# Performance work log

Hardware: AMD Instinct MI355X
Metric: run time of the kernel (lower is better)

The kernel has to match this reference:

```python
import jax, jax.numpy as jnp
import numpy as np

N_HEADS = 8
WINDOW = 7

def _conv1x1(x, W, b):
    # x: [B,H,W,C]; 1x1 conv == per-pixel matmul
    return jnp.einsum('bhwc,cd->bhwd', x, W) + b

def _to_heads(t, nh):
    # [B,H,W,C] -> channels-first reshape [B, nh, C//nh, H*W] (matches tf transpose+reshape)
    B, H, W, C = t.shape
    return jnp.transpose(t, (0, 3, 1, 2)).reshape(B, nh, C // nh, H * W)

def setup_inputs() -> dict:
    key = jax.random.key(0)
    ks = jax.random.split(key, 8)
    B, H, W, C = 2, 56, 56, 256
    x = jax.random.normal(ks[0], (B, H, W, C), dtype=jnp.float32)
    s = 1.0 / np.sqrt(C)
    Wq = jax.random.normal(ks[1], (C, C), dtype=jnp.float32) * s
    bq = jnp.zeros((C,), dtype=jnp.float32)
    Wk = jax.random.normal(ks[2], (C, C), dtype=jnp.float32) * s
    bk = jnp.zeros((C,), dtype=jnp.float32)
    Wv = jax.random.normal(ks[3], (C, C), dtype=jnp.float32) * s
    bv = jnp.zeros((C,), dtype=jnp.float32)
    # original initializes gamma to 0 (output == x); use small nonzero so the
    # attention path is observable in outputs/grads
    gamma = jax.random.normal(ks[4], (1,), dtype=jnp.float32) * 0.1
    return {"x": x, "Wq": Wq, "bq": bq, "Wk": Wk, "bk": bk, "Wv": Wv, "bv": bv, "gamma": gamma}

def reference(x, Wq, bq, Wk, bk, Wv, bv, gamma):
    B, H, W, C = x.shape
    p = WINDOW // 2
    xp = jnp.pad(x, ((0, 0), (p, p), (p, p), (0, 0)), mode='reflect')  # [B,Hp,Wp,C]
    q = _to_heads(_conv1x1(x, Wq, bq), N_HEADS)    # [B,nh,dk,HW]
    k = _to_heads(_conv1x1(xp, Wk, bk), N_HEADS)   # [B,nh,dk,HpWp]
    v = _to_heads(_conv1x1(xp, Wv, bv), N_HEADS)   # [B,nh,dk,HpWp]
    energy = jnp.einsum('bhdq,bhdk->bhqk', q, k)   # [B,nh,HW,HpWp]
    attn = jax.nn.softmax(energy, axis=-1)
    out = jnp.einsum('bhdk,bhqk->bhdq', v, attn)   # [B,nh,dk,HW]
    out = out.reshape(B, C, H, W).transpose(0, 2, 3, 1)
    return gamma * out + x
```

## Files before the change

### kernel.cpp

```cpp
#include <hip/hip_runtime.h>

typedef unsigned short u16;
typedef float f32x4 __attribute__((ext_vector_type(4)));
typedef short bf16x8 __attribute__((ext_vector_type(8)));
typedef short bf16x4 __attribute__((ext_vector_type(4)));

__device__ __forceinline__ u16 f2bf(float f) {
    unsigned u = __float_as_uint(f);
    u = (u + 0x7FFFu + ((u >> 16) & 1u)) >> 16;
    return (u16)u;
}

#define LOG2E 1.4426950408889634f

#if __has_builtin(__builtin_amdgcn_exp2f)
__device__ __forceinline__ float exp2_fast(float x) { return __builtin_amdgcn_exp2f(x); }
#else
__device__ __forceinline__ float exp2_fast(float x) { return __expf(x * 0.6931471805599453f); }
#endif

__device__ __forceinline__ unsigned pack2bf(float a, float b) {
    unsigned ua = __float_as_uint(a) + 0x8000u;
    unsigned ub = __float_as_uint(b) + 0x8000u;
#if __has_builtin(__builtin_amdgcn_perm)
    return __builtin_amdgcn_perm(ub, ua, 0x07060302u);
#else
    return ((ua >> 16) & 0xFFFFu) | (ub & 0xFFFF0000u);
#endif
}

#if __has_builtin(__builtin_amdgcn_cvt_pk_bf16_f32)
typedef __bf16 bf2_t __attribute__((ext_vector_type(2)));
__device__ __forceinline__ unsigned cvtpk(float a, float b) {
    bf2_t r = __builtin_amdgcn_cvt_pk_bf16_f32(a, b);
    return __builtin_bit_cast(unsigned, r);
}
#else
__device__ __forceinline__ unsigned cvtpk(float a, float b) { return pack2bf(a, b); }
#endif

__device__ __forceinline__ bf16x4 bc4(uint2 u) { return __builtin_bit_cast(bf16x4, u); }
__device__ __forceinline__ bf16x8 bc8(uint4 u) { return __builtin_bit_cast(bf16x8, u); }

#if __has_builtin(__builtin_amdgcn_global_load_lds)
typedef const __attribute__((address_space(1))) void* as1cv;
typedef __attribute__((address_space(3))) void* as3v;
__device__ __forceinline__ void dma16(const void* g, void* lds_base, int lane) {
    __builtin_amdgcn_global_load_lds((as1cv)g, (as3v)lds_base, 16, 0, 0);
}
#else
__device__ __forceinline__ void dma16(const void* g, void* lds_base, int lane) {
    *(uint4*)((char*)lds_base + lane * 16) = *(const uint4*)g;
}
#endif

#if __has_builtin(__builtin_amdgcn_mfma_f32_16x16x16bf16_1k)
__device__ __forceinline__ f32x4 pv_mfma(bf16x4 a, bf16x4 b, f32x4 c) {
    return __builtin_amdgcn_mfma_f32_16x16x16bf16_1k(a, b, c, 0, 0, 0);
}
#elif __has_builtin(__builtin_amdgcn_mfma_f32_16x16x16_bf16)
__device__ __forceinline__ f32x4 pv_mfma(bf16x4 a, bf16x4 b, f32x4 c) {
    return __builtin_amdgcn_mfma_f32_16x16x16_bf16(a, b, c, 0, 0, 0);
}
#else
__device__ __forceinline__ f32x4 pv_mfma(bf16x4 a, bf16x4 b, f32x4 c) {
    bf16x8 a8 = {a[0], a[1], a[2], a[3], 0, 0, 0, 0};
    bf16x8 b8 = {b[0], b[1], b[2], b[3], 0, 0, 0, 0};
    return __builtin_amdgcn_mfma_f32_16x16x32_bf16(a8, b8, c, 0, 0, 0);
}
#endif

#define BB 2
#define HH 56
#define CC 256
#define NH 8
#define DK 32
#define SQ 3136
#define HP 62
#define SK 3844
#define VT_STRIDE 3856

#define WS_Q    0
#define WS_K    1605632
#define WS_VT   3573760
#define WS_LB   5548032

#define NZERO_F4 413952

#define BSTR 40
__global__ __launch_bounds__(256, 4) void proj_kernel(const float* __restrict__ x,
                                                      const float* __restrict__ Wq,
                                                      const float* __restrict__ Wk,
                                                      const float* __restrict__ Wv,
                                                      const float* __restrict__ bq,
                                                      const float* __restrict__ bk,
                                                      const float* __restrict__ bv,
                                                      u16* __restrict__ qout,
                                                      u16* __restrict__ kout,
                                                      u16* __restrict__ vtout,
                                                      float* __restrict__ out,
                                                      float* __restrict__ lbuf) {
    __shared__ __align__(16) u16 Bl[128 * BSTR];

    int mode  = blockIdx.y;
    int nz    = blockIdx.z;
    int mbase = blockIdx.x * 64;
    int tid = threadIdx.x;

    {
        int gid = ((blockIdx.z * 3 + blockIdx.y) * 121 + blockIdx.x) * 256 + tid;
        const int n_out4 = (SQ * BB * CC) / 4;
        for (int i = gid; i < NZERO_F4; i += 726 * 256) {
            if (i < n_out4) *(float4*)&out[i * 4] = (float4){0.f, 0.f, 0.f, 0.f};
            else            *(float4*)&lbuf[(i - n_out4) * 4] = (float4){0.f, 0.f, 0.f, 0.f};
        }
    }

    int M = (mode == 0) ? (BB * SQ) : (BB * SK);
    if (mbase >= M) return;
    int wave = tid >> 6, lane = tid & 63, quad = lane >> 4, l16 = lane & 15;

    const float* W = (mode == 0) ? Wq : ((mode == 1) ? Wk : Wv);
    const float* bias = (mode == 0) ? bq : ((mode == 1) ? bk : bv);
    float wscale = (mode == 0) ? LOG2E : 1.0f;

    int m_a = mbase + wave * 16 + l16;
    if (m_a >= M) m_a = M - 1;
    int xrow;
    if (mode == 0) {
        xrow = m_a;
    } else {
        int b = (m_a >= SK) ? 1 : 0;
        int sp = m_a - b * SK;
        int hp = sp / HP, wp = sp - hp * HP;
        int hs = hp - 3; hs = hs < 0 ? -hs : (hs >= HH ? 110 - hs : hs);
        int ws_ = wp - 3; ws_ = ws_ < 0 ? -ws_ : (ws_ >= HH ? 110 - ws_ : ws_);
        xrow = b * SQ + hs * HH + ws_;
    }
    const float* xr = x + (size_t)xrow * 256;

    int kq = tid >> 3;
    int cb = (tid & 7) * 16;

    f32x4 acc[8];
#pragma unroll
    for (int i = 0; i < 8; i++) acc[i] = (f32x4){0.f, 0.f, 0.f, 0.f};

    float4 wreg[4];
    auto wload = [&](int s) {
        const float* p = W + (size_t)(s * 32 + kq) * 256 + nz * 128 + cb;
        wreg[0] = *(const float4*)&p[0];
        wreg[1] = *(const float4*)&p[4];
        wreg[2] = *(const float4*)&p[8];
        wreg[3] = *(const float4*)&p[12];
    };

    wload(0);
    for (int s = 0; s < 8; ++s) {
        int kk = s * 32;
#pragma unroll
        for (int i = 0; i < 16; i++) {
            float v = ((const float*)wreg)[i] * wscale;
            Bl[(cb + i) * BSTR + kq] = f2bf(v);
        }
        __syncthreads();
        if (s < 7) wload(s + 1);
        float4 f0 = *(const float4*)&xr[kk + quad * 8];
        float4 f1 = *(const float4*)&xr[kk + quad * 8 + 4];
        uint4 aw = (uint4){pack2bf(f0.x, f0.y), pack2bf(f0.z, f0.w),
                           pack2bf(f1.x, f1.y), pack2bf(f1.z, f1.w)};
        bf16x8 afrag = bc8(aw);
#pragma unroll
        for (int nt = 0; nt < 8; nt++) {
            bf16x8 bfrag = *(const bf16x8*)&Bl[(nt * 16 + l16) * BSTR + quad * 8];
            acc[nt] = __builtin_amdgcn_mfma_f32_16x16x32_bf16(afrag, bfrag, acc[nt], 0, 0, 0);
        }
        __syncthreads();
    }

    int mrow_base = mbase + wave * 16 + quad * 4;
    if (mode == 2) {
#pragma unroll
        for (int nt = 0; nt < 8; nt++) {
            int c = nz * 128 + nt * 16 + l16;
            float bvv = bias[c];
#pragma unroll
            for (int p = 0; p < 4; p += 2) {
                int m = mrow_base + p;
                if (m + 1 < M) {
                    int bb = (m >= SK) ? 1 : 0;
                    int kp = m - bb * SK;
                    unsigned pk = pack2bf(acc[nt][p] + bvv, acc[nt][p + 1] + bvv);
                    *(unsigned*)&vtout[(size_t)(bb * 256 + c) * VT_STRIDE + kp] = pk;
                }
            }
        }
    } else {
#pragma unroll
        for (int r = 0; r < 4; r++) {
            int m = mrow_base + r;
            if (m >= M) continue;
#pragma unroll
            for (int nt = 0; nt < 8; nt++) {
                int c = nz * 128 + nt * 16 + l16;
                float v = acc[nt][r] + bias[c] * ((mode == 0) ? LOG2E : 1.0f);
                u16 hv = f2bf(v);
                if (mode == 0) qout[((size_t)m << 8) + c] = hv;
                else           kout[((size_t)m << 8) + c] = hv;
            }
        }
    }
}

__global__ __launch_bounds__(256, 4) void attn_kernel(const u16* __restrict__ qb,
                                                      const u16* __restrict__ kb,
                                                      const u16* __restrict__ vtb,
                                                      float* __restrict__ out,
                                                      float* __restrict__ lbuf) {
    __shared__ __align__(16) u16 S[16384];

    int tid = threadIdx.x;
    int th = tid >> 6, lane = tid & 63, quad = lane >> 4, l16 = lane & 15;
    int bh = blockIdx.y;
    int b = bh >> 3, h = bh & 7;
    int half = blockIdx.z;
    int qsub = blockIdx.x * 64;
    int rounds = half ? 15 : 16;

    bf16x8 qf[4];
#pragma unroll
    for (int i = 0; i < 4; ++i)
        qf[i] = *(const bf16x8*)&qb[((size_t)(b * SQ + qsub + i * 16 + l16) << 8) + h * 32 + quad * 8];

    const u16* kg = kb + ((size_t)(b * SK) << 8) + h * 32;
    const u16* vg = vtb + (size_t)(b * 256 + h * 32) * VT_STRIDE;

    f32x4 o[4][2], lv[4];
#pragma unroll
    for (int i = 0; i < 4; ++i) {
        o[i][0] = (f32x4){0.f,0.f,0.f,0.f};
        o[i][1] = (f32x4){0.f,0.f,0.f,0.f};
        lv[i]   = (f32x4){0.f,0.f,0.f,0.f};
    }

    short ov = (l16 == 0) ? (short)0x3F80 : (short)0;
    bf16x4 ones4 = {ov, ov, ov, ov};

    auto stage = [&](int r_ch, int buf) {
        u16* base = &S[buf * 8192];
        int kbase = (half * 16 + r_ch) * 128;
#pragma unroll
        for (int i = 0; i < 2; ++i) {
            int g = th + i * 4;
            int grow = kbase + g * 16 + (lane & 15);
            if (grow > SK - 1) grow = SK - 1;
            dma16(kg + ((size_t)grow << 8) + (lane >> 4) * 8, base + g * 512, lane);
            int col = kbase + (2 * g + (lane >> 5)) * 8;
            if (col > VT_STRIDE - 8) col = VT_STRIDE - 8;
            dma16(vg + (size_t)(lane & 31) * VT_STRIDE + col, base + 4096 + g * 512, lane);
        }
    };

    stage(0, 0);
    __syncthreads();
    stage(1, 1);

    for (int r = 0; r < rounds; ++r) {
        const u16* Kl = &S[(r & 1) * 8192];
        const u16* Vl = Kl + 4096;
        int ch = half * 16 + r;
        bool tail = (ch == 30);
#pragma unroll
        for (int tt = 0; tt < 2; ++tt) {
            int t = th + tt * 4;
            bf16x8 kf = *(const bf16x8*)&Kl[t * 512 + ((quad << 4) + l16) * 8];
            f32x4 e[4];
#pragma unroll
            for (int i = 0; i < 4; ++i)
                e[i] = __builtin_amdgcn_mfma_f32_16x16x32_bf16(kf, qf[i], (f32x4){0.f,0.f,0.f,0.f}, 0, 0, 0);
            bf16x4 pa[4];
            if (tail) {
                int kb0 = ch * 128 + t * 16 + quad * 4;
#pragma unroll
                for (int i = 0; i < 4; ++i) {
                    float p0 = (kb0 + 0) < SK ? exp2_fast(e[i][0]) : 0.f;
                    float p1 = (kb0 + 1) < SK ? exp2_fast(e[i][1]) : 0.f;
                    float p2 = (kb0 + 2) < SK ? exp2_fast(e[i][2]) : 0.f;
                    float p3 = (kb0 + 3) < SK ? exp2_fast(e[i][3]) : 0.f;
                    pa[i] = bc4((uint2){cvtpk(p0, p1), cvtpk(p2, p3)});
                }
            } else {
#pragma unroll
                for (int i = 0; i < 4; ++i) {
                    pa[i] = bc4((uint2){cvtpk(exp2_fast(e[i][0]), exp2_fast(e[i][1])),
                                        cvtpk(exp2_fast(e[i][2]), exp2_fast(e[i][3]))});
                }
            }
            int vbase = ((2 * t + (quad >> 1)) << 8) + (quad & 1) * 4;
            uint2 w0 = *(const uint2*)&Vl[vbase + l16 * 8];
            uint2 w1 = *(const uint2*)&Vl[vbase + (16 + l16) * 8];
            bf16x4 vb0 = bc4(w0), vb1 = bc4(w1);
#pragma unroll
            for (int i = 0; i < 4; ++i) {
                o[i][0] = pv_mfma(pa[i], vb0, o[i][0]);
                o[i][1] = pv_mfma(pa[i], vb1, o[i][1]);
                lv[i]   = pv_mfma(pa[i], ones4, lv[i]);
            }
        }
        __syncthreads();
        if (r + 2 < rounds) stage(r + 2, r & 1);
    }

    float* mg = (float*)&S[0];
    {
        int slot = ((th & 1) * 64 + lane) * 48;
        if (th >= 2) {
#pragma unroll
            for (int i = 0; i < 4; ++i) {
                *(f32x4*)&mg[slot + i * 8]     = o[i][0];
                *(f32x4*)&mg[slot + i * 8 + 4] = o[i][1];
                *(f32x4*)&mg[slot + 32 + i * 4] = lv[i];
            }
        }
        __syncthreads();
        if (th < 2) {
#pragma unroll
            for (int i = 0; i < 4; ++i) {
                o[i][0] += *(const f32x4*)&mg[slot + i * 8];
                o[i][1] += *(const f32x4*)&mg[slot + i * 8 + 4];
                lv[i]   += *(const f32x4*)&mg[slot + 32 + i * 4];
            }
        }
        __syncthreads();
    }
    {
        int slot = lane * 48;
        if (th == 1) {
#pragma unroll
            for (int i = 0; i < 4; ++i) {
                *(f32x4*)&mg[slot + i * 8]     = o[i][0];
                *(f32x4*)&mg[slot + i * 8 + 4] = o[i][1];
                *(f32x4*)&mg[slot + 32 + i * 4] = lv[i];
            }
        }
        __syncthreads();
        if (th == 0) {
#pragma unroll
            for (int i = 0; i < 4; ++i) {
                o[i][0] += *(const f32x4*)&mg[slot + i * 8];
                o[i][1] += *(const f32x4*)&mg[slot + i * 8 + 4];
                lv[i]   += *(const f32x4*)&mg[slot + 32 + i * 4];
            }

#pragma unroll
            for (int i = 0; i < 4; ++i) {
#pragma unroll
                for (int r2 = 0; r2 < 4; ++r2) {
                    int q = qsub + i * 16 + quad * 4 + r2;
                    size_t base = (size_t)(b * SQ + q) * 256 + h * 32;
                    atomicAdd(&out[base + l16],      o[i][0][r2]);
                    atomicAdd(&out[base + 16 + l16], o[i][1][r2]);
                    if (l16 == 0) atomicAdd(&lbuf[(b * SQ + q) * 8 + h], lv[i][r2]);
                }
            }
        }
    }
}

__global__ __launch_bounds__(256) void finalize_kernel(const float* __restrict__ x,
                                                       const float* __restrict__ gammap,
                                                       const float* __restrict__ lbuf,
                                                       float* __restrict__ out) {
    int gid = blockIdx.x * 256 + threadIdx.x;
    int row = gid >> 6;
    int c4  = (gid & 63) << 2;
    int h   = c4 >> 5;
    float g = gammap[0];
    float linv = g / lbuf[row * 8 + h];
    size_t base = (size_t)row * 256 + c4;
    float4 o = *(const float4*)&out[base];
    float4 xv = *(const float4*)&x[base];
    o.x = o.x * linv + xv.x;
    o.y = o.y * linv + xv.y;
    o.z = o.z * linv + xv.z;
    o.w = o.w * linv + xv.w;
    *(float4*)&out[base] = o;
}

extern "C" void kernel_launch(void* const* d_in, const int* in_sizes, int n_in,
                              void* d_out, int out_size, void* d_ws, size_t ws_size,
                              hipStream_t stream) {
    const float* x     = (const float*)d_in[0];
    const float* Wq    = (const float*)d_in[1];
    const float* bq    = (const float*)d_in[2];
    const float* Wk    = (const float*)d_in[3];
    const float* bk    = (const float*)d_in[4];
    const float* Wv    = (const float*)d_in[5];
    const float* bv    = (const float*)d_in[6];
    const float* gamma = (const float*)d_in[7];
    float* out = (float*)d_out;

    u16* ws   = (u16*)d_ws;
    u16* qbuf = ws + WS_Q;
    u16* kbuf = ws + WS_K;
    u16* vtb  = ws + WS_VT;
    float* lbuf = (float*)(ws + WS_LB);

    proj_kernel<<<dim3(121, 3, 2), 256, 0, stream>>>(x, Wq, Wk, Wv, bq, bk, bv,
                                                     qbuf, kbuf, vtb, out, lbuf);
    attn_kernel<<<dim3(49, 16, 2), 256, 0, stream>>>(qbuf, kbuf, vtb, out, lbuf);
    finalize_kernel<<<1568, 256, 0, stream>>>(x, gamma, lbuf, out);
}
```

Baseline: 155.7 us.

## Pretranspose weights, drop KV split and atomics, fuse finalize into attention

Adds a weight-prep kernel that converts and transposes Wq/Wk/Wv to bf16 once, so the projection kernel reads B fragments straight from global memory with no LDS staging or barriers. The attention kernel stops splitting keys into two halves, so each block processes all 31 chunks and writes the normalized, gamma-scaled residual output directly. This removes the zeroing pass, the atomics and the finalize kernel. The PV product now uses 16x16x32 MFMAs by packing two key tiles, and the row sum is computed with VALU adds instead of an extra MFMA against ones. The cost is half as many attention blocks (784) and therefore less parallelism, plus one extra small launch.

```diff
diff --git a/kernel.cpp b/kernel.cpp
--- a/kernel.cpp
+++ b/kernel.cpp
@@ -3,7 +3,7 @@
 typedef unsigned short u16;
 typedef float f32x4 __attribute__((ext_vector_type(4)));
 typedef short bf16x8 __attribute__((ext_vector_type(8)));
-typedef short bf16x4 __attribute__((ext_vector_type(4)));
+typedef u16 u16x4 __attribute__((ext_vector_type(4)));
 
 __device__ __forceinline__ u16 f2bf(float f) {
     unsigned u = __float_as_uint(f);
@@ -39,7 +39,6 @@
 __device__ __forceinline__ unsigned cvtpk(float a, float b) { return pack2bf(a, b); }
 #endif
 
-__device__ __forceinline__ bf16x4 bc4(uint2 u) { return __builtin_bit_cast(bf16x4, u); }
 __device__ __forceinline__ bf16x8 bc8(uint4 u) { return __builtin_bit_cast(bf16x8, u); }
 
 #if __has_builtin(__builtin_amdgcn_global_load_lds)
@@ -54,27 +53,8 @@
 }
 #endif
 
-#if __has_builtin(__builtin_amdgcn_mfma_f32_16x16x16bf16_1k)
-__device__ __forceinline__ f32x4 pv_mfma(bf16x4 a, bf16x4 b, f32x4 c) {
-    return __builtin_amdgcn_mfma_f32_16x16x16bf16_1k(a, b, c, 0, 0, 0);
-}
-#elif __has_builtin(__builtin_amdgcn_mfma_f32_16x16x16_bf16)
-__device__ __forceinline__ f32x4 pv_mfma(bf16x4 a, bf16x4 b, f32x4 c) {
-    return __builtin_amdgcn_mfma_f32_16x16x16_bf16(a, b, c, 0, 0, 0);
-}
-#else
-__device__ __forceinline__ f32x4 pv_mfma(bf16x4 a, bf16x4 b, f32x4 c) {
-    bf16x8 a8 = {a[0], a[1], a[2], a[3], 0, 0, 0, 0};
-    bf16x8 b8 = {b[0], b[1], b[2], b[3], 0, 0, 0, 0};
-    return __builtin_amdgcn_mfma_f32_16x16x32_bf16(a8, b8, c, 0, 0, 0);
-}
-#endif
-
 #define BB 2
 #define HH 56
-#define CC 256
-#define NH 8
-#define DK 32
 #define SQ 3136
 #define HP 62
 #define SK 3844
@@ -83,46 +63,61 @@
 #define WS_Q    0
 #define WS_K    1605632
 #define WS_VT   3573760
-#define WS_LB   5548032
-
-#define NZERO_F4 413952
-
-#define BSTR 40
+#define WS_WT   5548032
+
+__global__ __launch_bounds__(256) void wprep_kernel(const float* __restrict__ Wq,
+                                                    const float* __restrict__ Wk,
+                                                    const float* __restrict__ Wv,
+                                                    u16* __restrict__ wt,
+                                                    u16* __restrict__ vtb) {
+    __shared__ u16 T[64][72];
+    int m = blockIdx.z;
+    const float* W = (m == 0) ? Wq : ((m == 1) ? Wk : Wv);
+    float sc = (m == 0) ? LOG2E : 1.0f;
+    int kx = blockIdx.x * 64, dx = blockIdx.y * 64;
+    int tid = threadIdx.x;
+    int r16 = tid >> 4, c4 = (tid & 15) * 4;
+#pragma unroll
+    for (int p = 0; p < 4; ++p) {
+        int kr = p * 16 + r16;
+        float4 f = *(const float4*)&W[(size_t)(kx + kr) * 256 + dx + c4];
+        T[c4 + 0][kr] = f2bf(f.x * sc);
+        T[c4 + 1][kr] = f2bf(f.y * sc);
+        T[c4 + 2][kr] = f2bf(f.z * sc);
+        T[c4 + 3][kr] = f2bf(f.w * sc);
+    }
+    __syncthreads();
+#pragma unroll
+    for (int p = 0; p < 4; ++p) {
+        int dr = p * 16 + r16;
+        u16x4 v = {T[dr][c4], T[dr][c4 + 1], T[dr][c4 + 2], T[dr][c4 + 3]};
+        *(u16x4*)&wt[(size_t)m * 65536 + (size_t)(dx + dr) * 256 + kx + c4] = v;
+    }
+    if (m == 0 && blockIdx.x == 0 && blockIdx.y == 0) {
+        for (int i = tid; i < 512 * 12; i += 256) {
+            int row = i / 12, col = 3844 + (i - row * 12);
+            vtb[(size_t)row * VT_STRIDE + col] = 0;
+        }
+    }
+}
+
 __global__ __launch_bounds__(256, 4) void proj_kernel(const float* __restrict__ x,
-                                                      const float* __restrict__ Wq,
-                                                      const float* __restrict__ Wk,
-                                                      const float* __restrict__ Wv,
+                                                      const u16* __restrict__ wt,
                                                       const float* __restrict__ bq,
                                                       const float* __restrict__ bk,
                                                       const float* __restrict__ bv,
                                                       u16* __restrict__ qout,
                                                       u16* __restrict__ kout,
-                                                      u16* __restrict__ vtout,
-                                                      float* __restrict__ out,
-                                                      float* __restrict__ lbuf) {
-    __shared__ __align__(16) u16 Bl[128 * BSTR];
-
-    int mode  = blockIdx.y;
-    int nz    = blockIdx.z;
+                                                      u16* __restrict__ vtout) {
+    int mode = blockIdx.y, nz = blockIdx.z;
     int mbase = blockIdx.x * 64;
-    int tid = threadIdx.x;
-
-    {
-        int gid = ((blockIdx.z * 3 + blockIdx.y) * 121 + blockIdx.x) * 256 + tid;
-        const int n_out4 = (SQ * BB * CC) / 4;
-        for (int i = gid; i < NZERO_F4; i += 726 * 256) {
-            if (i < n_out4) *(float4*)&out[i * 4] = (float4){0.f, 0.f, 0.f, 0.f};
-            else            *(float4*)&lbuf[(i - n_out4) * 4] = (float4){0.f, 0.f, 0.f, 0.f};
-        }
-    }
-
     int M = (mode == 0) ? (BB * SQ) : (BB * SK);
     if (mbase >= M) return;
-    int wave = tid >> 6, lane = tid & 63, quad = lane >> 4, l16 = lane & 15;
-
-    const float* W = (mode == 0) ? Wq : ((mode == 1) ? Wk : Wv);
+    int tid = threadIdx.x;
+    int wave = tid >> 6, quad = (tid >> 4) & 3, l16 = tid & 15;
     const float* bias = (mode == 0) ? bq : ((mode == 1) ? bk : bv);
-    float wscale = (mode == 0) ? LOG2E : 1.0f;
+    const u16* Wm = wt + (size_t)mode * 65536 + (size_t)(nz * 128) * 256;
+    const u16* wr = Wm + (size_t)l16 * 256 + quad * 8;
 
     int m_a = mbase + wave * 16 + l16;
     if (m_a >= M) m_a = M - 1;
@@ -130,52 +125,31 @@
     if (mode == 0) {
         xrow = m_a;
     } else {
-        int b = (m_a >= SK) ? 1 : 0;
-        int sp = m_a - b * SK;
+        int bb = (m_a >= SK) ? 1 : 0;
+        int sp = m_a - bb * SK;
         int hp = sp / HP, wp = sp - hp * HP;
         int hs = hp - 3; hs = hs < 0 ? -hs : (hs >= HH ? 110 - hs : hs);
         int ws_ = wp - 3; ws_ = ws_ < 0 ? -ws_ : (ws_ >= HH ? 110 - ws_ : ws_);
-        xrow = b * SQ + hs * HH + ws_;
+        xrow = bb * SQ + hs * HH + ws_;
     }
     const float* xr = x + (size_t)xrow * 256;
 
-    int kq = tid >> 3;
-    int cb = (tid & 7) * 16;
-
     f32x4 acc[8];
 #pragma unroll
     for (int i = 0; i < 8; i++) acc[i] = (f32x4){0.f, 0.f, 0.f, 0.f};
 
-    float4 wreg[4];
-    auto wload = [&](int s) {
-        const float* p = W + (size_t)(s * 32 + kq) * 256 + nz * 128 + cb;
-        wreg[0] = *(const float4*)&p[0];
-        wreg[1] = *(const float4*)&p[4];
-        wreg[2] = *(const float4*)&p[8];
-        wreg[3] = *(const float4*)&p[12];
-    };
-
-    wload(0);
+#pragma unroll
     for (int s = 0; s < 8; ++s) {
-        int kk = s * 32;
-#pragma unroll
-        for (int i = 0; i < 16; i++) {
-            float v = ((const float*)wreg)[i] * wscale;
-            Bl[(cb + i) * BSTR + kq] = f2bf(v);
-        }
-        __syncthreads();
-        if (s < 7) wload(s + 1);
-        float4 f0 = *(const float4*)&xr[kk + quad * 8];
-        float4 f1 = *(const float4*)&xr[kk + quad * 8 + 4];
+        float4 f0 = *(const float4*)&xr[s * 32 + quad * 8];
+        float4 f1 = *(const float4*)&xr[s * 32 + quad * 8 + 4];
         uint4 aw = (uint4){pack2bf(f0.x, f0.y), pack2bf(f0.z, f0.w),
                            pack2bf(f1.x, f1.y), pack2bf(f1.z, f1.w)};
-        bf16x8 afrag = bc8(aw);
+        bf16x8 af = bc8(aw);
 #pragma unroll
         for (int nt = 0; nt < 8; nt++) {
-            bf16x8 bfrag = *(const bf16x8*)&Bl[(nt * 16 + l16) * BSTR + quad * 8];
-            acc[nt] = __builtin_amdgcn_mfma_f32_16x16x32_bf16(afrag, bfrag, acc[nt], 0, 0, 0);
-        }
-        __syncthreads();
+            bf16x8 bfrag = *(const bf16x8*)&wr[nt * 4096 + s * 32];
+            acc[nt] = __builtin_amdgcn_mfma_f32_16x16x32_bf16(af, bfrag, acc[nt], 0, 0, 0);
+        }
     }
 
     int mrow_base = mbase + wave * 16 + quad * 4;
@@ -215,17 +189,16 @@
 __global__ __launch_bounds__(256, 4) void attn_kernel(const u16* __restrict__ qb,
                                                       const u16* __restrict__ kb,
                                                       const u16* __restrict__ vtb,
-                                                      float* __restrict__ out,
-                                                      float* __restrict__ lbuf) {
+                                                      const float* __restrict__ x,
+                                                      const float* __restrict__ gammap,
+                                                      float* __restrict__ out) {
     __shared__ __align__(16) u16 S[16384];
 
     int tid = threadIdx.x;
     int th = tid >> 6, lane = tid & 63, quad = lane >> 4, l16 = lane & 15;
-    int bh = blockIdx.y;
+    int bh = blockIdx.x;
     int b = bh >> 3, h = bh & 7;
-    int half = blockIdx.z;
-    int qsub = blockIdx.x * 64;
-    int rounds = half ? 15 : 16;
+    int qsub = blockIdx.y * 64;
 
     bf16x8 qf[4];
 #pragma unroll
@@ -235,20 +208,17 @@
     const u16* kg = kb + ((size_t)(b * SK) << 8) + h * 32;
     const u16* vg = vtb + (size_t)(b * 256 + h * 32) * VT_STRIDE;
 
-    f32x4 o[4][2], lv[4];
+    f32x4 o[4][2];
+    f32x4 lacc = (f32x4){0.f, 0.f, 0.f, 0.f};
 #pragma unroll
     for (int i = 0; i < 4; ++i) {
-        o[i][0] = (f32x4){0.f,0.f,0.f,0.f};
-        o[i][1] = (f32x4){0.f,0.f,0.f,0.f};
-        lv[i]   = (f32x4){0.f,0.f,0.f,0.f};
-    }
-
-    short ov = (l16 == 0) ? (short)0x3F80 : (short)0;
-    bf16x4 ones4 = {ov, ov, ov, ov};
+        o[i][0] = (f32x4){0.f, 0.f, 0.f, 0.f};
+        o[i][1] = (f32x4){0.f, 0.f, 0.f, 0.f};
+    }
 
     auto stage = [&](int r_ch, int buf) {
         u16* base = &S[buf * 8192];
-        int kbase = (half * 16 + r_ch) * 128;
+        int kbase = r_ch * 128;
 #pragma unroll
         for (int i = 0; i < 2; ++i) {
             int g = th + i * 4;
@@ -265,62 +235,65 @@
     __syncthreads();
     stage(1, 1);
 
-    for (int r = 0; r < rounds; ++r) {
+    int tA = th, tB = th + 4;
+    int vOffA = tA * 512 + (((quad >> 1) * 32 + l16) << 3) + (quad & 1) * 4;
+    int vOffB = tB * 512 + (((quad >> 1) * 32 + l16) << 3) + (quad & 1) * 4;
+
+    for (int r = 0; r < 31; ++r) {
         const u16* Kl = &S[(r & 1) * 8192];
         const u16* Vl = Kl + 4096;
-        int ch = half * 16 + r;
-        bool tail = (ch == 30);
-#pragma unroll
-        for (int tt = 0; tt < 2; ++tt) {
-            int t = th + tt * 4;
-            bf16x8 kf = *(const bf16x8*)&Kl[t * 512 + ((quad << 4) + l16) * 8];
-            f32x4 e[4];
-#pragma unroll
-            for (int i = 0; i < 4; ++i)
-                e[i] = __builtin_amdgcn_mfma_f32_16x16x32_bf16(kf, qf[i], (f32x4){0.f,0.f,0.f,0.f}, 0, 0, 0);
-            bf16x4 pa[4];
+        bf16x8 kfA = *(const bf16x8*)&Kl[tA * 512 + lane * 8];
+        bf16x8 kfB = *(const bf16x8*)&Kl[tB * 512 + lane * 8];
+        uint2 wA0 = *(const uint2*)&Vl[vOffA];
+        uint2 wB0 = *(const uint2*)&Vl[vOffB];
+        uint2 wA1 = *(const uint2*)&Vl[vOffA + 128];
+        uint2 wB1 = *(const uint2*)&Vl[vOffB + 128];
+        bf16x8 V0 = bc8((uint4){wA0.x, wA0.y, wB0.x, wB0.y});
+        bf16x8 V1 = bc8((uint4){wA1.x, wA1.y, wB1.x, wB1.y});
+
+        f32x4 eA[4], eB[4];
+#pragma unroll
+        for (int i = 0; i < 4; ++i)
+            eA[i] = __builtin_amdgcn_mfma_f32_16x16x32_bf16(kfA, qf[i], (f32x4){0.f, 0.f, 0.f, 0.f}, 0, 0, 0);
+#pragma unroll
+        for (int i = 0; i < 4; ++i)
+            eB[i] = __builtin_amdgcn_mfma_f32_16x16x32_bf16(kfB, qf[i], (f32x4){0.f, 0.f, 0.f, 0.f}, 0, 0, 0);
+
+        bool tail = (r == 30);
+#pragma unroll
+        for (int i = 0; i < 4; ++i) {
+            float pA0 = exp2_fast(eA[i][0]), pA1 = exp2_fast(eA[i][1]);
+            float pA2 = exp2_fast(eA[i][2]), pA3 = exp2_fast(eA[i][3]);
+            float pB0 = exp2_fast(eB[i][0]), pB1 = exp2_fast(eB[i][1]);
+            float pB2 = exp2_fast(eB[i][2]), pB3 = exp2_fast(eB[i][3]);
             if (tail) {
-                int kb0 = ch * 128 + t * 16 + quad * 4;
-#pragma unroll
-                for (int i = 0; i < 4; ++i) {
-                    float p0 = (kb0 + 0) < SK ? exp2_fast(e[i][0]) : 0.f;
-                    float p1 = (kb0 + 1) < SK ? exp2_fast(e[i][1]) : 0.f;
-                    float p2 = (kb0 + 2) < SK ? exp2_fast(e[i][2]) : 0.f;
-                    float p3 = (kb0 + 3) < SK ? exp2_fast(e[i][3]) : 0.f;
-                    pa[i] = bc4((uint2){cvtpk(p0, p1), cvtpk(p2, p3)});
-                }
-            } else {
-#pragma unroll
-                for (int i = 0; i < 4; ++i) {
-                    pa[i] = bc4((uint2){cvtpk(exp2_fast(e[i][0]), exp2_fast(e[i][1])),
-                                        cvtpk(exp2_fast(e[i][2]), exp2_fast(e[i][3]))});
-                }
-            }
-            int vbase = ((2 * t + (quad >> 1)) << 8) + (quad & 1) * 4;
-            uint2 w0 = *(const uint2*)&Vl[vbase + l16 * 8];
-            uint2 w1 = *(const uint2*)&Vl[vbase + (16 + l16) * 8];
-            bf16x4 vb0 = bc4(w0), vb1 = bc4(w1);
-#pragma unroll
-            for (int i = 0; i < 4; ++i) {
-                o[i][0] = pv_mfma(pa[i], vb0, o[i][0]);
-                o[i][1] = pv_mfma(pa[i], vb1, o[i][1]);
-                lv[i]   = pv_mfma(pa[i], ones4, lv[i]);
-            }
+                int kA0 = 3840 + tA * 16 + quad * 4;
+                pA0 = (kA0 + 0 < SK) ? pA0 : 0.f;
+                pA1 = (kA0 + 1 < SK) ? pA1 : 0.f;
+                pA2 = (kA0 + 2 < SK) ? pA2 : 0.f;
+                pA3 = (kA0 + 3 < SK) ? pA3 : 0.f;
+                pB0 = 0.f; pB1 = 0.f; pB2 = 0.f; pB3 = 0.f;
+            }
+            lacc[i] += ((pA0 + pA1) + (pA2 + pA3)) + ((pB0 + pB1) + (pB2 + pB3));
+            bf16x8 pa = bc8((uint4){cvtpk(pA0, pA1), cvtpk(pA2, pA3),
+                                    cvtpk(pB0, pB1), cvtpk(pB2, pB3)});
+            o[i][0] = __builtin_amdgcn_mfma_f32_16x16x32_bf16(pa, V0, o[i][0], 0, 0, 0);
+            o[i][1] = __builtin_amdgcn_mfma_f32_16x16x32_bf16(pa, V1, o[i][1], 0, 0, 0);
         }
         __syncthreads();
-        if (r + 2 < rounds) stage(r + 2, r & 1);
+        if (r + 2 < 31) stage(r + 2, r & 1);
     }
 
     float* mg = (float*)&S[0];
     {
-        int slot = ((th & 1) * 64 + lane) * 48;
+        int slot = ((th & 1) * 64 + lane) * 40;
         if (th >= 2) {
 #pragma unroll
             for (int i = 0; i < 4; ++i) {
                 *(f32x4*)&mg[slot + i * 8]     = o[i][0];
                 *(f32x4*)&mg[slot + i * 8 + 4] = o[i][1];
-                *(f32x4*)&mg[slot + 32 + i * 4] = lv[i];
-            }
+            }
+            *(f32x4*)&mg[slot + 32] = lacc;
         }
         __syncthreads();
         if (th < 2) {
@@ -328,20 +301,20 @@
             for (int i = 0; i < 4; ++i) {
                 o[i][0] += *(const f32x4*)&mg[slot + i * 8];
                 o[i][1] += *(const f32x4*)&mg[slot + i * 8 + 4];
-                lv[i]   += *(const f32x4*)&mg[slot + 32 + i * 4];
-            }
+            }
+            lacc += *(const f32x4*)&mg[slot + 32];
         }
         __syncthreads();
     }
     {
-        int slot = lane * 48;
+        int slot = lane * 40;
         if (th == 1) {
 #pragma unroll
             for (int i = 0; i < 4; ++i) {
                 *(f32x4*)&mg[slot + i * 8]     = o[i][0];
                 *(f32x4*)&mg[slot + i * 8 + 4] = o[i][1];
-                *(f32x4*)&mg[slot + 32 + i * 4] = lv[i];
-            }
+            }
+            *(f32x4*)&mg[slot + 32] = lacc;
         }
         __syncthreads();
         if (th == 0) {
@@ -349,42 +322,30 @@
             for (int i = 0; i < 4; ++i) {
                 o[i][0] += *(const f32x4*)&mg[slot + i * 8];
                 o[i][1] += *(const f32x4*)&mg[slot + i * 8 + 4];
-                lv[i]   += *(const f32x4*)&mg[slot + 32 + i * 4];
-            }
-
+            }
+            lacc += *(const f32x4*)&mg[slot + 32];
+#pragma unroll
+            for (int c = 0; c < 4; ++c) {
+                float v = lacc[c];
+                v += __shfl_xor(v, 16);
+                v += __shfl_xor(v, 32);
+                lacc[c] = v;
+            }
+            float g = gammap[0];
 #pragma unroll
             for (int i = 0; i < 4; ++i) {
 #pragma unroll
                 for (int r2 = 0; r2 < 4; ++r2) {
+                    float l = __shfl(lacc[i], quad * 4 + r2);
+                    float scl = g / l;
                     int q = qsub + i * 16 + quad * 4 + r2;
-                    size_t base = (size_t)(b * SQ + q) * 256 + h * 32;
-                    atomicAdd(&out[base + l16],      o[i][0][r2]);
-                    atomicAdd(&out[base + 16 + l16], o[i][1][r2]);
-                    if (l16 == 0) atomicAdd(&lbuf[(b * SQ + q) * 8 + h], lv[i][r2]);
+                    size_t base = ((size_t)(b * SQ + q) << 8) + h * 32 + l16;
+                    out[base]      = o[i][0][r2] * scl + x[base];
+                    out[base + 16] = o[i][1][r2] * scl + x[base + 16];
                 }
             }
         }
     }
-}
-
-__global__ __launch_bounds__(256) void finalize_kernel(const float* __restrict__ x,
-                                                       const float* __restrict__ gammap,
-                                                       const float* __restrict__ lbuf,
-                                                       float* __restrict__ out) {
-    int gid = blockIdx.x * 256 + threadIdx.x;
-    int row = gid >> 6;
-    int c4  = (gid & 63) << 2;
-    int h   = c4 >> 5;
-    float g = gammap[0];
-    float linv = g / lbuf[row * 8 + h];
-    size_t base = (size_t)row * 256 + c4;
-    float4 o = *(const float4*)&out[base];
-    float4 xv = *(const float4*)&x[base];
-    o.x = o.x * linv + xv.x;
-    o.y = o.y * linv + xv.y;
-    o.z = o.z * linv + xv.z;
-    o.w = o.w * linv + xv.w;
-    *(float4*)&out[base] = o;
 }
 
 extern "C" void kernel_launch(void* const* d_in, const int* in_sizes, int n_in,
@@ -404,10 +365,9 @@
     u16* qbuf = ws + WS_Q;
     u16* kbuf = ws + WS_K;
     u16* vtb  = ws + WS_VT;
-    float* lbuf = (float*)(ws + WS_LB);
-
-    proj_kernel<<<dim3(121, 3, 2), 256, 0, stream>>>(x, Wq, Wk, Wv, bq, bk, bv,
-                                                     qbuf, kbuf, vtb, out, lbuf);
-    attn_kernel<<<dim3(49, 16, 2), 256, 0, stream>>>(qbuf, kbuf, vtb, out, lbuf);
-    finalize_kernel<<<1568, 256, 0, stream>>>(x, gamma, lbuf, out);
-}
+    u16* wt   = ws + WS_WT;
+
+    wprep_kernel<<<dim3(4, 4, 3), 256, 0, stream>>>(Wq, Wk, Wv, wt, vtb);
+    proj_kernel<<<dim3(121, 3, 2), 256, 0, stream>>>(x, wt, bq, bk, bv, qbuf, kbuf, vtb);
+    attn_kernel<<<dim3(16, 49), 256, 0, stream>>>(qbuf, kbuf, vtb, x, gamma, out);
+}
```

Measured after the change: 166.5 us. 1.07x slower.
